# Optimization experiments

Measured on AMD Instinct MI355X. Metric: run time of the kernel, lower is better.

## Reference

```python
import jax, jax.numpy as jnp
import numpy as np

B, S, D, H = 2, 4096, 512, 8
DK = D // H  # 64


def setup_inputs() -> dict:
    key = jax.random.key(0)
    ks = jax.random.split(key, 7)
    scale = 1.0 / np.sqrt(D)
    return {
        "query": jax.random.normal(ks[0], (B, S, D), dtype=jnp.float32),
        "key": jax.random.normal(ks[1], (B, S, D), dtype=jnp.float32),
        "value": jax.random.normal(ks[2], (B, S, D), dtype=jnp.float32),
        # nn.Linear weights, stored [out, in] as in torch; y = x @ W.T
        "Wq": jax.random.normal(ks[3], (D, D), dtype=jnp.float32) * scale,
        "Wk": jax.random.normal(ks[4], (D, D), dtype=jnp.float32) * scale,
        "Wv": jax.random.normal(ks[5], (D, D), dtype=jnp.float32) * scale,
        "Wo": jax.random.normal(ks[6], (D, D), dtype=jnp.float32) * scale,
    }


def reference(query, key, value, Wq, Wk, Wv, Wo):
    # projections (torch Linear: x @ W.T)
    q = query @ Wq.T  # [B,S,D]
    k = key @ Wk.T
    v = value @ Wv.T
    # split heads -> [B,H,S,DK]
    q = q.reshape(B, S, H, DK).transpose(0, 2, 1, 3)
    k = k.reshape(B, S, H, DK).transpose(0, 2, 1, 3)
    v = v.reshape(B, S, H, DK).transpose(0, 2, 1, 3)
    # scores [B,H,S,S], softmax, weighted sum (dropout=0 / eval)
    scores = jnp.einsum("bhqd,bhkd->bhqk", q, k) / np.sqrt(DK).astype(np.float32)
    weights = jax.nn.softmax(scores, axis=-1)
    attn = jnp.einsum("bhqk,bhkd->bhqd", weights, v)  # [B,H,S,DK]
    # merge heads -> [B,S,D], output projection
    out = attn.transpose(0, 2, 1, 3).reshape(B, S, D)
    return out @ Wo.T
```

## Files before the change

kernel.cpp:

```cpp
#include <hip/hip_runtime.h>
#include <hip/hip_bf16.h>

typedef short short8 __attribute__((ext_vector_type(8)));
typedef short short4v __attribute__((ext_vector_type(4)));
typedef float floatx4 __attribute__((ext_vector_type(4)));
typedef unsigned int uint4v __attribute__((ext_vector_type(4)));

constexpr int Bc = 2, Sc = 4096, Dc = 512, Hc = 8, DKc = 64;
constexpr int Mc = Bc * Sc;

static __device__ __forceinline__ unsigned short f2bf(float f) {
  unsigned int u = __builtin_bit_cast(unsigned int, f);
  unsigned int rb = ((u >> 16) & 1u) + 0x7fffu;
  return (unsigned short)((u + rb) >> 16);
}
static __device__ __forceinline__ unsigned int cvt_pk_bf16(float lo, float hi) {
  unsigned int r;
  asm("v_cvt_pk_bf16_f32 %0, %1, %2" : "=v"(r) : "v"(lo), "v"(hi));
  return r;
}
static __device__ __forceinline__ float exp2_fast(float x) {
  float r;
  asm("v_exp_f32 %0, %1" : "=v"(r) : "v"(x));
  return r;
}

template <int IN_F32, int OUT_F32, int W_F32>
static __device__ __forceinline__ void gemm_body(
    const void* __restrict__ Xv, const void* __restrict__ Wp,
    void* __restrict__ Yv, const int N, const int K) {
  constexpr int BM = 128, BN = 64, BK = 32, LDP = 40;
  __shared__ unsigned short As[2][BM * LDP];
  __shared__ unsigned short Bs[2][BN * LDP];
  const int tid = threadIdx.x;
  const int lane = tid & 63, wid = tid >> 6;
  const int wm = wid >> 1, wn = wid & 1;
  const int bm = blockIdx.y * BM, bn = blockIdx.x * BN;
  const int rq = lane & 15, kk8 = (lane >> 4) * 8;
  const int sr = tid >> 1, sc = (tid & 1) * 16;
  const int brow = tid >> 2, bc8 = (tid & 3) * 8;

  floatx4 acc[4][2] = {};

  float a32[16];
  short8 a16[2];
  float b32[8];
  short8 b16;

  auto load_tile = [&](int k0) {
    if (IN_F32) {
      const float* src = (const float*)Xv + (size_t)(bm + sr) * K + k0 + sc;
#pragma unroll
      for (int i = 0; i < 4; ++i) {
        float4 v = *(const float4*)(src + i * 4);
        a32[4 * i + 0] = v.x; a32[4 * i + 1] = v.y;
        a32[4 * i + 2] = v.z; a32[4 * i + 3] = v.w;
      }
    } else {
      const unsigned short* src =
          (const unsigned short*)Xv + (size_t)(bm + sr) * K + k0 + sc;
      a16[0] = *(const short8*)src;
      a16[1] = *(const short8*)(src + 8);
    }
    if (W_F32) {
      const float* wsrc = (const float*)Wp + (size_t)(bn + brow) * K + k0 + bc8;
#pragma unroll
      for (int i = 0; i < 2; ++i) {
        float4 v = *(const float4*)(wsrc + i * 4);
        b32[4 * i + 0] = v.x; b32[4 * i + 1] = v.y;
        b32[4 * i + 2] = v.z; b32[4 * i + 3] = v.w;
      }
    } else {
      b16 = *(const short8*)((const unsigned short*)Wp +
                             (size_t)(bn + brow) * K + k0 + bc8);
    }
  };
  auto store_tile = [&](int bf) {
    if (IN_F32) {
      unsigned int t2[8];
#pragma unroll
      for (int i = 0; i < 8; ++i) t2[i] = cvt_pk_bf16(a32[2 * i], a32[2 * i + 1]);
      uint4v u0 = {t2[0], t2[1], t2[2], t2[3]};
      uint4v u1 = {t2[4], t2[5], t2[6], t2[7]};
      *(uint4v*)&As[bf][sr * LDP + sc] = u0;
      *(uint4v*)&As[bf][sr * LDP + sc + 8] = u1;
    } else {
      *(short8*)&As[bf][sr * LDP + sc] = a16[0];
      *(short8*)&As[bf][sr * LDP + sc + 8] = a16[1];
    }
    if (W_F32) {
      unsigned int t2[4];
#pragma unroll
      for (int i = 0; i < 4; ++i) t2[i] = cvt_pk_bf16(b32[2 * i], b32[2 * i + 1]);
      uint4v u = {t2[0], t2[1], t2[2], t2[3]};
      *(uint4v*)&Bs[bf][brow * LDP + bc8] = u;
    } else {
      *(short8*)&Bs[bf][brow * LDP + bc8] = b16;
    }
  };

  load_tile(0);
  store_tile(0);

  const int NK = K / BK;
  for (int it = 0; it < NK; ++it) {
    const int cur = it & 1;
    __syncthreads();

    if (it < NK - 1) load_tile((it + 1) * BK);

    short8 af[4], bfr[2];
#pragma unroll
    for (int mi = 0; mi < 4; ++mi)
      af[mi] = *(const short8*)&As[cur][(wm * 64 + mi * 16 + rq) * LDP + kk8];
#pragma unroll
    for (int ni = 0; ni < 2; ++ni)
      bfr[ni] = *(const short8*)&Bs[cur][(wn * 32 + ni * 16 + rq) * LDP + kk8];
#pragma unroll
    for (int mi = 0; mi < 4; ++mi)
#pragma unroll
      for (int ni = 0; ni < 2; ++ni)
        acc[mi][ni] = __builtin_amdgcn_mfma_f32_16x16x32_bf16(
            af[mi], bfr[ni], acc[mi][ni], 0, 0, 0);

    if (it < NK - 1) store_tile(cur ^ 1);
  }

#pragma unroll
  for (int mi = 0; mi < 4; ++mi)
#pragma unroll
    for (int ni = 0; ni < 2; ++ni)
#pragma unroll
      for (int j = 0; j < 4; ++j) {
        int r = bm + wm * 64 + mi * 16 + (lane >> 4) * 4 + j;
        int c = bn + wn * 32 + ni * 16 + rq;
        float v = acc[mi][ni][j];
        if (OUT_F32)
          ((float*)Yv)[(size_t)r * N + c] = v;
        else
          ((unsigned short*)Yv)[(size_t)r * N + c] = f2bf(v);
      }
}

__global__ __launch_bounds__(256) void gemm_qkv(
    const float* __restrict__ xq, const float* __restrict__ xk,
    const float* __restrict__ xv, const float* __restrict__ wq,
    const float* __restrict__ wk, const float* __restrict__ wv,
    unsigned short* __restrict__ yq, unsigned short* __restrict__ yk,
    unsigned short* __restrict__ yv) {
  const int z = blockIdx.z;
  const float* X = (z == 0) ? xq : (z == 1) ? xk : xv;
  const float* W = (z == 0) ? wq : (z == 1) ? wk : wv;
  unsigned short* Y = (z == 0) ? yq : (z == 1) ? yk : yv;
  gemm_body<1, 0, 1>(X, W, Y, Dc, Dc);
}

__global__ __launch_bounds__(256) void gemm_out(
    const unsigned short* __restrict__ x, const float* __restrict__ w,
    float* __restrict__ y) {
  gemm_body<0, 1, 1>(x, w, y, Dc, Dc);
}

__global__ __launch_bounds__(256) void transpose_v(
    const unsigned short* __restrict__ vb, unsigned short* __restrict__ vt) {
  constexpr int LDT = 65;
  __shared__ unsigned short T[64 * LDT];
  const int tid = threadIdx.x;
  const int s0 = blockIdx.x * 64, c0 = blockIdx.y * 64, b = blockIdx.z;
  const int r = tid >> 2, cs = (tid & 3) * 16;
  const unsigned short* src = vb + ((size_t)b * Sc + s0 + r) * Dc + c0 + cs;
  *(short8*)&T[r * LDT + cs] = *(const short8*)src;
  *(short8*)&T[r * LDT + cs + 8] = *(const short8*)(src + 8);
  __syncthreads();
  unsigned short tmp[16];
#pragma unroll
  for (int j = 0; j < 16; ++j) tmp[j] = T[(cs + j) * LDT + r];
  const int k4 = (cs >> 4) & 1;
  const int base32 = s0 + (cs & 32);
  unsigned short* dstrow = vt + ((size_t)b * Dc + c0 + r) * Sc;
#pragma unroll
  for (int g = 0; g < 4; ++g) {
    short4v v4 = {(short)tmp[4 * g + 0], (short)tmp[4 * g + 1],
                  (short)tmp[4 * g + 2], (short)tmp[4 * g + 3]};
    *(short4v*)(dstrow + base32 + g * 8 + k4 * 4) = v4;
  }
}

__global__ __launch_bounds__(512, 4) void attn_fwd(
    const unsigned short* __restrict__ Qp, const unsigned short* __restrict__ Kp,
    const unsigned short* __restrict__ Vtp, unsigned short* __restrict__ Op) {
  __shared__ unsigned char smem[33792];
  unsigned short* KsB = (unsigned short*)smem;
  unsigned short* VsB = (unsigned short*)(smem + 16384);

  const int tid = threadIdx.x, lane = tid & 63, wid = tid >> 6;
  const int qc = wid >> 1, kh = wid & 1;
  const int b = blockIdx.y >> 3, h = blockIdx.y & 7;
  const int q0 = blockIdx.x * 128 + qc * 32;
  const int rq = lane & 15, lg = lane >> 4, kk8 = lg * 8;

  const unsigned short* Qb = Qp + ((size_t)b * Sc) * Dc + h * DKc;
  const unsigned short* Kb = Kp + ((size_t)b * Sc) * Dc + h * DKc;
  const unsigned short* Vh = Vtp + ((size_t)b * Dc + h * DKc) * Sc;

  short8 qa[2][2];
#pragma unroll
  for (int qi = 0; qi < 2; ++qi)
#pragma unroll
    for (int c = 0; c < 2; ++c)
      qa[qi][c] = *(const short8*)(Qb + (size_t)(q0 + qi * 16 + rq) * Dc + c * 32 + kk8);

  floatx4 o_acc[2][4] = {};
  floatx4 acc_l[2] = {};
  float m_run[2] = {-1e30f, -1e30f};

  short8 ones;
#pragma unroll
  for (int j = 0; j < 8; ++j) ones[j] = (short)0x3F80;

  const float C2 = 0.18033688f;
  const float THR = 8.0f;

  const int sr = tid >> 3, sc8 = (tid & 7) * 8;
  const int st = (sr * 64 + sc8) ^ ((sr & 7) << 3);
  const int sx = (rq & 7) << 3;

  short8 kr = *(const short8*)(Kb + (size_t)sr * Dc + sc8);
  short8 vr = *(const short8*)(Vh + (size_t)sr * Sc + sc8);
  *(short8*)&KsB[st] = kr;
  *(short8*)&VsB[st] = vr;

  for (int it = 0; it < 64; ++it) {
    const int cur = it & 1;
    __syncthreads();

    if (it < 63) {
      const int kn = (it + 1) * 64;
      kr = *(const short8*)(Kb + (size_t)(kn + sr) * Dc + sc8);
      vr = *(const short8*)(Vh + (size_t)sr * Sc + kn + sc8);
    }

    const unsigned short* Ks = KsB + cur * 4096;
    const unsigned short* Vs = VsB + cur * 4096;

    short8 ka[2][2];
#pragma unroll
    for (int ks = 0; ks < 2; ++ks)
#pragma unroll
      for (int c = 0; c < 2; ++c) {
        const int row = kh * 32 + ks * 16 + rq;
        ka[ks][c] = *(const short8*)&Ks[(row * 64 + c * 32 + kk8) ^ sx];
      }

    short8 pb_[2];
#pragma unroll
    for (int qi = 0; qi < 2; ++qi) {
      floatx4 s[2] = {};
#pragma unroll
      for (int ks = 0; ks < 2; ++ks) {
        s[ks] = __builtin_amdgcn_mfma_f32_16x16x32_bf16(ka[ks][0], qa[qi][0], s[ks], 0, 0, 0);
        s[ks] = __builtin_amdgcn_mfma_f32_16x16x32_bf16(ka[ks][1], qa[qi][1], s[ks], 0, 0, 0);
      }
      float t1 = fmaxf(fmaxf(s[0][0], s[0][1]), s[0][2]);
      float t2 = fmaxf(fmaxf(s[0][3], s[1][0]), s[1][1]);
      float t3 = fmaxf(fmaxf(s[1][2], s[1][3]), t1);
      float tp = fmaxf(t3, t2) * C2;

      if (__any(tp > m_run[qi] + THR)) {
        float tm = tp;
        tm = fmaxf(tm, __shfl_xor(tm, 16, 64));
        tm = fmaxf(tm, __shfl_xor(tm, 32, 64));
        if (__any(tm > m_run[qi])) {
          float mn = fmaxf(m_run[qi], tm);
          float scf = exp2_fast(m_run[qi] - mn);
          m_run[qi] = mn;
          float sc_c[4];
#pragma unroll
          for (int j = 0; j < 4; ++j) sc_c[j] = __shfl(scf, lg * 4 + j, 64);
#pragma unroll
          for (int j = 0; j < 4; ++j) {
            acc_l[qi][j] *= sc_c[j];
#pragma unroll
            for (int dt = 0; dt < 4; ++dt) o_acc[qi][dt][j] *= sc_c[j];
          }
        }
      }

      const float lm = m_run[qi];
      unsigned int pw0, pw1, pw2, pw3;
      {
        float p0 = exp2_fast(fmaf(s[0][0], C2, -lm));
        float p1 = exp2_fast(fmaf(s[0][1], C2, -lm));
        float p2 = exp2_fast(fmaf(s[0][2], C2, -lm));
        float p3 = exp2_fast(fmaf(s[0][3], C2, -lm));
        pw0 = cvt_pk_bf16(p0, p1);
        pw1 = cvt_pk_bf16(p2, p3);
      }
      {
        float p0 = exp2_fast(fmaf(s[1][0], C2, -lm));
        float p1 = exp2_fast(fmaf(s[1][1], C2, -lm));
        float p2 = exp2_fast(fmaf(s[1][2], C2, -lm));
        float p3 = exp2_fast(fmaf(s[1][3], C2, -lm));
        pw2 = cvt_pk_bf16(p0, p1);
        pw3 = cvt_pk_bf16(p2, p3);
      }
      uint4v pw = {pw0, pw1, pw2, pw3};
      pb_[qi] = __builtin_bit_cast(short8, pw);
    }

#pragma unroll
    for (int dt = 0; dt < 4; ++dt) {
      const int vrow = dt * 16 + rq;
      short8 v = *(const short8*)&Vs[(vrow * 64 + kh * 32 + kk8) ^ sx];
      o_acc[0][dt] = __builtin_amdgcn_mfma_f32_16x16x32_bf16(pb_[0], v, o_acc[0][dt], 0, 0, 0);
      o_acc[1][dt] = __builtin_amdgcn_mfma_f32_16x16x32_bf16(pb_[1], v, o_acc[1][dt], 0, 0, 0);
    }
    acc_l[0] = __builtin_amdgcn_mfma_f32_16x16x32_bf16(pb_[0], ones, acc_l[0], 0, 0, 0);
    acc_l[1] = __builtin_amdgcn_mfma_f32_16x16x32_bf16(pb_[1], ones, acc_l[1], 0, 0, 0);

    if (it < 63) {
      *(short8*)&KsB[(cur ^ 1) * 4096 + st] = kr;
      *(short8*)&VsB[(cur ^ 1) * 4096 + st] = vr;
    }
  }

  __syncthreads();
  float* MO = (float*)smem;
  float* ML = (float*)(smem + 32768);
  if (kh == 1) {
#pragma unroll
    for (int qi = 0; qi < 2; ++qi) {
#pragma unroll
      for (int j = 0; j < 4; ++j) {
        int row = qc * 32 + qi * 16 + lg * 4 + j;
        if (rq == 0) ML[row * 2 + 1] = acc_l[qi][j];
#pragma unroll
        for (int dt = 0; dt < 4; ++dt)
          MO[(size_t)row * 64 + dt * 16 + rq] = o_acc[qi][dt][j];
      }
      if (lg == 0) ML[(qc * 32 + qi * 16 + rq) * 2] = m_run[qi];
    }
  }
  __syncthreads();
  if (kh == 0) {
#pragma unroll
    for (int qi = 0; qi < 2; ++qi) {
      float m0c[4];
#pragma unroll
      for (int j = 0; j < 4; ++j) m0c[j] = __shfl(m_run[qi], lg * 4 + j, 64);
#pragma unroll
      for (int j = 0; j < 4; ++j) {
        int row = qc * 32 + qi * 16 + lg * 4 + j;
        int r = q0 + qi * 16 + lg * 4 + j;
        float m1 = ML[row * 2 + 0], l1 = ML[row * 2 + 1];
        float mx = fmaxf(m0c[j], m1);
        float a0 = exp2_fast(m0c[j] - mx), a1 = exp2_fast(m1 - mx);
        float inv = 1.0f / (acc_l[qi][j] * a0 + l1 * a1);
#pragma unroll
        for (int dt = 0; dt < 4; ++dt) {
          float o = (o_acc[qi][dt][j] * a0 + MO[(size_t)row * 64 + dt * 16 + rq] * a1) * inv;
          Op[((size_t)b * Sc + r) * Dc + h * DKc + dt * 16 + rq] = f2bf(o);
        }
      }
    }
  }
}

extern "C" void kernel_launch(void* const* d_in, const int* in_sizes, int n_in,
                              void* d_out, int out_size, void* d_ws, size_t ws_size,
                              hipStream_t stream) {
  const float* q_in = (const float*)d_in[0];
  const float* k_in = (const float*)d_in[1];
  const float* v_in = (const float*)d_in[2];
  const float* Wq = (const float*)d_in[3];
  const float* Wk = (const float*)d_in[4];
  const float* Wv = (const float*)d_in[5];
  const float* Wo = (const float*)d_in[6];

  unsigned short* qb = (unsigned short*)d_ws;
  unsigned short* kb = qb + (size_t)Mc * Dc;
  unsigned short* vb = kb + (size_t)Mc * Dc;
  unsigned short* ab = vb + (size_t)Mc * Dc;
  unsigned short* vt = ab + (size_t)Mc * Dc;

  dim3 gq(Dc / 64, Mc / 128, 3);
  gemm_qkv<<<gq, 256, 0, stream>>>(q_in, k_in, v_in, Wq, Wk, Wv, qb, kb, vb);

  dim3 tg(Sc / 64, Dc / 64, Bc);
  transpose_v<<<tg, 256, 0, stream>>>(vb, vt);

  dim3 ga(Sc / 128, Bc * Hc);
  attn_fwd<<<ga, 512, 0, stream>>>(qb, kb, vt, ab);

  dim3 gg(Dc / 64, Mc / 128);
  gemm_out<<<gg, 256, 0, stream>>>(ab, Wo, (float*)d_out);
}
```

Before: 172.0 us.

## Fuse V transpose into QKV GEMM epilogue and remap attention block order

The V projection GEMM now writes its output directly in the transposed Vt layout, staging the tile through shared memory, so the separate transpose_v kernel and its extra round trip through global memory are removed. The attention kernel also remaps its block index so that consecutive blocks are spread across batch-heads, which changes how blocks are scheduled and which K/V data is resident in cache at the same time. The cost is two extra barriers and an LDS staging pass in the V GEMM epilogue.

```diff
diff --git a/kernel.cpp b/kernel.cpp
--- a/kernel.cpp
+++ b/kernel.cpp
@@ -25,7 +25,7 @@
   return r;
 }
 
-template <int IN_F32, int OUT_F32, int W_F32>
+template <int IN_F32, int OUT_F32, int W_F32, int VT_OUT>
 static __device__ __forceinline__ void gemm_body(
     const void* __restrict__ Xv, const void* __restrict__ Wp,
     void* __restrict__ Yv, const int N, const int K) {
@@ -36,7 +36,7 @@
   const int lane = tid & 63, wid = tid >> 6;
   const int wm = wid >> 1, wn = wid & 1;
   const int bm = blockIdx.y * BM, bn = blockIdx.x * BN;
-  const int rq = lane & 15, kk8 = (lane >> 4) * 8;
+  const int rq = lane & 15, lg = lane >> 4, kk8 = lg * 8;
   const int sr = tid >> 1, sc = (tid & 1) * 16;
   const int brow = tid >> 2, bc8 = (tid & 3) * 8;
 
@@ -126,20 +126,45 @@
     if (it < NK - 1) store_tile(cur ^ 1);
   }
 
-#pragma unroll
-  for (int mi = 0; mi < 4; ++mi)
-#pragma unroll
-    for (int ni = 0; ni < 2; ++ni)
-#pragma unroll
-      for (int j = 0; j < 4; ++j) {
-        int r = bm + wm * 64 + mi * 16 + (lane >> 4) * 4 + j;
-        int c = bn + wn * 32 + ni * 16 + rq;
-        float v = acc[mi][ni][j];
-        if (OUT_F32)
-          ((float*)Yv)[(size_t)r * N + c] = v;
-        else
-          ((unsigned short*)Yv)[(size_t)r * N + c] = f2bf(v);
-      }
+  if (VT_OUT) {
+    __syncthreads();
+    unsigned short* T = (unsigned short*)As;
+    const int bb = bm >> 12;
+    const int sl0 = bm & 4095;
+#pragma unroll
+    for (int mi = 0; mi < 4; ++mi) {
+      const int spb = wm * 64 + (mi >> 1) * 32 + lg * 8 + (mi & 1) * 4;
+#pragma unroll
+      for (int ni = 0; ni < 2; ++ni) {
+        const int c = wn * 32 + ni * 16 + rq;
+#pragma unroll
+        for (int j = 0; j < 4; ++j)
+          T[c * 136 + spb + j] = f2bf(acc[mi][ni][j]);
+      }
+    }
+    __syncthreads();
+    const int c = tid >> 2, seg = (tid & 3) * 32;
+    unsigned short* dst = (unsigned short*)Yv +
+        ((size_t)bb * Dc + bn + c) * Sc + sl0 + seg;
+#pragma unroll
+    for (int u = 0; u < 4; ++u)
+      *(short8*)(dst + u * 8) = *(const short8*)&T[c * 136 + seg + u * 8];
+  } else {
+#pragma unroll
+    for (int mi = 0; mi < 4; ++mi)
+#pragma unroll
+      for (int ni = 0; ni < 2; ++ni)
+#pragma unroll
+        for (int j = 0; j < 4; ++j) {
+          int r = bm + wm * 64 + mi * 16 + lg * 4 + j;
+          int c = bn + wn * 32 + ni * 16 + rq;
+          float v = acc[mi][ni][j];
+          if (OUT_F32)
+            ((float*)Yv)[(size_t)r * N + c] = v;
+          else
+            ((unsigned short*)Yv)[(size_t)r * N + c] = f2bf(v);
+        }
+  }
 }
 
 __global__ __launch_bounds__(256) void gemm_qkv(
@@ -147,43 +172,22 @@
     const float* __restrict__ xv, const float* __restrict__ wq,
     const float* __restrict__ wk, const float* __restrict__ wv,
     unsigned short* __restrict__ yq, unsigned short* __restrict__ yk,
-    unsigned short* __restrict__ yv) {
+    unsigned short* __restrict__ vt) {
   const int z = blockIdx.z;
-  const float* X = (z == 0) ? xq : (z == 1) ? xk : xv;
-  const float* W = (z == 0) ? wq : (z == 1) ? wk : wv;
-  unsigned short* Y = (z == 0) ? yq : (z == 1) ? yk : yv;
-  gemm_body<1, 0, 1>(X, W, Y, Dc, Dc);
+  if (z == 2) {
+    gemm_body<1, 0, 1, 1>(xv, wv, vt, Dc, Dc);
+  } else {
+    const float* X = (z == 0) ? xq : xk;
+    const float* W = (z == 0) ? wq : wk;
+    unsigned short* Y = (z == 0) ? yq : yk;
+    gemm_body<1, 0, 1, 0>(X, W, Y, Dc, Dc);
+  }
 }
 
 __global__ __launch_bounds__(256) void gemm_out(
     const unsigned short* __restrict__ x, const float* __restrict__ w,
     float* __restrict__ y) {
-  gemm_body<0, 1, 1>(x, w, y, Dc, Dc);
-}
-
-__global__ __launch_bounds__(256) void transpose_v(
-    const unsigned short* __restrict__ vb, unsigned short* __restrict__ vt) {
-  constexpr int LDT = 65;
-  __shared__ unsigned short T[64 * LDT];
-  const int tid = threadIdx.x;
-  const int s0 = blockIdx.x * 64, c0 = blockIdx.y * 64, b = blockIdx.z;
-  const int r = tid >> 2, cs = (tid & 3) * 16;
-  const unsigned short* src = vb + ((size_t)b * Sc + s0 + r) * Dc + c0 + cs;
-  *(short8*)&T[r * LDT + cs] = *(const short8*)src;
-  *(short8*)&T[r * LDT + cs + 8] = *(const short8*)(src + 8);
-  __syncthreads();
-  unsigned short tmp[16];
-#pragma unroll
-  for (int j = 0; j < 16; ++j) tmp[j] = T[(cs + j) * LDT + r];
-  const int k4 = (cs >> 4) & 1;
-  const int base32 = s0 + (cs & 32);
-  unsigned short* dstrow = vt + ((size_t)b * Dc + c0 + r) * Sc;
-#pragma unroll
-  for (int g = 0; g < 4; ++g) {
-    short4v v4 = {(short)tmp[4 * g + 0], (short)tmp[4 * g + 1],
-                  (short)tmp[4 * g + 2], (short)tmp[4 * g + 3]};
-    *(short4v*)(dstrow + base32 + g * 8 + k4 * 4) = v4;
-  }
+  gemm_body<0, 1, 1, 0>(x, w, y, Dc, Dc);
 }
 
 __global__ __launch_bounds__(512, 4) void attn_fwd(
@@ -195,8 +199,11 @@
 
   const int tid = threadIdx.x, lane = tid & 63, wid = tid >> 6;
   const int qc = wid >> 1, kh = wid & 1;
-  const int b = blockIdx.y >> 3, h = blockIdx.y & 7;
-  const int q0 = blockIdx.x * 128 + qc * 32;
+  const int F = blockIdx.y * 32 + blockIdx.x;
+  const int L = (F & 7) * 64 + (F >> 3);
+  const int bh = L >> 5, qt = L & 31;
+  const int b = bh >> 3, h = bh & 7;
+  const int q0 = qt * 128 + qc * 32;
   const int rq = lane & 15, lg = lane >> 4, kk8 = lg * 8;
 
   const unsigned short* Qb = Qp + ((size_t)b * Sc) * Dc + h * DKc;
@@ -379,15 +386,11 @@
 
   unsigned short* qb = (unsigned short*)d_ws;
   unsigned short* kb = qb + (size_t)Mc * Dc;
-  unsigned short* vb = kb + (size_t)Mc * Dc;
-  unsigned short* ab = vb + (size_t)Mc * Dc;
+  unsigned short* ab = kb + (size_t)Mc * Dc;
   unsigned short* vt = ab + (size_t)Mc * Dc;
 
   dim3 gq(Dc / 64, Mc / 128, 3);
-  gemm_qkv<<<gq, 256, 0, stream>>>(q_in, k_in, v_in, Wq, Wk, Wv, qb, kb, vb);
-
-  dim3 tg(Sc / 64, Dc / 64, Bc);
-  transpose_v<<<tg, 256, 0, stream>>>(vb, vt);
+  gemm_qkv<<<gq, 256, 0, stream>>>(q_in, k_in, v_in, Wq, Wk, Wv, qb, kb, vt);
 
   dim3 ga(Sc / 128, Bc * Hc);
   attn_fwd<<<ga, 512, 0, stream>>>(qb, kb, vt, ab);
```

Measured after the change: 162.9 us (median of 2 runs). 5.3% less time.
